# Optimization experiments

Measured on AMD Instinct MI355X. Metric: run time of the kernel, lower is better.

The kernel has to match this reference:

```python
import jax, jax.numpy as jnp
import numpy as np

E = 8       # n_experts
K = 2       # k_experts
D_IN = 1024
D_OUT = 1024
D_EXP = 2048
N = 16384   # tokens (batch*seq, forward requires 2D input)


def setup_inputs() -> dict:
    key = jax.random.key(0)
    ks = jax.random.split(key, 4)
    x = jax.random.normal(ks[0], (N, D_IN), jnp.float32)
    Wg = jax.random.normal(ks[1], (E, D_IN), jnp.float32) * 0.02      # router weight
    bg = jnp.zeros((E,), jnp.float32)                                  # router bias
    W_in = jax.random.normal(ks[2], (E, D_EXP, D_IN), jnp.float32) * 0.02
    b_in = jnp.zeros((E, D_EXP), jnp.float32)                          # w_in_bias_init=0.0
    W_out = jax.random.normal(ks[3], (E, D_OUT, D_EXP), jnp.float32) * 0.02  # bias=False
    return {"x": x, "Wg": Wg, "bg": bg, "W_in": W_in, "b_in": b_in, "W_out": W_out}


def moe_forward(x, Wg, bg, W_in, b_in, W_out):
    # Eval mode: gate jitter / solu jitter / dropouts are training-only no-ops.
    n = x.shape[0]
    # --- routing ---
    logits = x @ Wg.T + bg                                 # [N, E]
    probs = jax.nn.softmax(logits, axis=-1)
    mean_probs = probs.mean(axis=0)                        # [E]
    k_vals, k_idx = jax.lax.top_k(probs, K)                # [N, K]
    k_w = k_vals / k_vals.sum(axis=-1, keepdims=True)      # renormalized gate weights
    counts = jnp.bincount(k_idx.reshape(-1), length=E)     # [E] int
    load_balancing_loss = E * jnp.sum((counts.astype(x.dtype) / n) * mean_probs)
    # --- dispatch + expert w_in (loop over fixed small E; combine with one-hot mask) ---
    sel = jax.nn.one_hot(k_idx, E, dtype=x.dtype)          # [N, K, E]
    h = jnp.zeros((n, K, D_EXP), x.dtype)                  # preacts per (token, slot)
    for e in range(E):
        he = x @ W_in[e].T + b_in[e]                       # [N, D_EXP]
        h = h + sel[:, :, e][..., None] * he[:, None, :]
    # --- SoLU (eval): softmax(preacts) * preacts over hidden dim ---
    acts = jax.nn.softmax(h, axis=-1) * h                  # [N, K, D_EXP]
    # --- expert w_out (no bias) ---
    out = jnp.zeros((n, K, D_OUT), x.dtype)
    for e in range(E):
        oe = jnp.einsum('nkh,oh->nko', acts, W_out[e])
        out = out + sel[:, :, e][..., None] * oe
    # --- weighted combine over the K chosen experts ---
    outputs = (out * k_w[..., None]).sum(axis=1)           # [N, D_OUT]
    return outputs, load_balancing_loss


def reference(x, Wg, bg, W_in, b_in, W_out):
    return moe_forward(x, Wg, bg, W_in, b_in, W_out)
```

## Files before the change

### kernel.cpp

```cpp
#include <hip/hip_runtime.h>
#include <hip/hip_bf16.h>
#include <stdint.h>

#define E_EXP 8
#define NTOK  16384
#define DIN   1024
#define DEXP  2048
#define DOUT  1024
#define NSLOT (NTOK*2)
#define MAXT  264

#define AS_T  (128*64)
#define BS_T  (256*64)

typedef __attribute__((ext_vector_type(8))) short short8;
typedef __attribute__((ext_vector_type(8))) unsigned short ushort8;
typedef __attribute__((ext_vector_type(4))) unsigned short ushort4v;
typedef __attribute__((ext_vector_type(4))) float f32x4;

__device__ __forceinline__ unsigned short f2bf(float f){
  union { float f; uint32_t u; } v; v.f = f;
  uint32_t r = (v.u + 0x7FFFu + ((v.u >> 16) & 1u)) >> 16;
  return (unsigned short)r;
}
__device__ __forceinline__ float bf2f(unsigned short u){
  union { uint32_t u; float f; } v; v.u = ((uint32_t)u) << 16;
  return v.f;
}

__device__ __forceinline__ void async16(const void* g, void* l){
  __builtin_amdgcn_global_load_lds(
      (const __attribute__((address_space(1))) void*)g,
      (__attribute__((address_space(3))) void*)l, 16, 0, 0);
}

#define VMCNT12() asm volatile("s_waitcnt vmcnt(12)" ::: "memory")
#define VMCNT6()  asm volatile("s_waitcnt vmcnt(6)"  ::: "memory")
#define VMCNT0()  asm volatile("s_waitcnt vmcnt(0)"  ::: "memory")
#define BARRIER() do { asm volatile("" ::: "memory"); __builtin_amdgcn_s_barrier(); asm volatile("" ::: "memory"); } while(0)

__global__ __launch_bounds__(256) void cast2(const float* __restrict__ a,
                                             const float* __restrict__ b,
                                             unsigned short* __restrict__ da,
                                             unsigned short* __restrict__ db,
                                             int na, int nb){
  int i = (blockIdx.x*256 + threadIdx.x)*8;
  const float* s; unsigned short* d;
  if (i < na){ s = a + i; d = da + i; }
  else { int j = i - na; if (j >= nb) return; s = b + j; d = db + j; }
  float4 x = *(const float4*)(s);
  float4 y = *(const float4*)(s+4);
  ushort8 o;
  o[0]=f2bf(x.x); o[1]=f2bf(x.y); o[2]=f2bf(x.z); o[3]=f2bf(x.w);
  o[4]=f2bf(y.x); o[5]=f2bf(y.y); o[6]=f2bf(y.z); o[7]=f2bf(y.w);
  *(ushort8*)d = o;
}

__global__ __launch_bounds__(256) void router(
    const float* __restrict__ x, const float* __restrict__ Wg, const float* __restrict__ bg,
    unsigned short* __restrict__ xb,
    int* __restrict__ eidx, float* __restrict__ gw,
    int* __restrict__ counts, float* __restrict__ probsum)
{
  __shared__ float sWg[E_EXP*DIN];
  __shared__ float sps[E_EXP];
  __shared__ int   scnt[E_EXP];
  const int tid = threadIdx.x;
  for (int i = tid; i < E_EXP*DIN; i += 256) sWg[i] = Wg[i];
  if (tid < E_EXP){ sps[tid]=0.f; scnt[tid]=0; }
  __syncthreads();
  const int lane = tid & 63;
  const int wv   = tid >> 6;
  for (int it = 0; it < 16; ++it){
    const int token = blockIdx.x*64 + wv*16 + it;
    float4 xv[4];
#pragma unroll
    for (int j=0;j<4;++j) xv[j] = *(const float4*)&x[(size_t)token*DIN + j*256 + lane*4];
#pragma unroll
    for (int j=0;j<4;++j){
      ushort4v o;
      o[0]=f2bf(xv[j].x); o[1]=f2bf(xv[j].y); o[2]=f2bf(xv[j].z); o[3]=f2bf(xv[j].w);
      *(ushort4v*)&xb[(size_t)token*DIN + j*256 + lane*4] = o;
    }
    float p[E_EXP];
#pragma unroll
    for (int e2=0;e2<E_EXP;++e2){
      float s = 0.f;
#pragma unroll
      for (int j=0;j<4;++j){
        const float4 w4 = *(const float4*)&sWg[e2*DIN + j*256 + lane*4];
        s += xv[j].x*w4.x + xv[j].y*w4.y + xv[j].z*w4.z + xv[j].w*w4.w;
      }
      p[e2] = s;
    }
#pragma unroll
    for (int d=1; d<64; d<<=1){
#pragma unroll
      for (int e2=0;e2<E_EXP;++e2) p[e2] += __shfl_xor(p[e2], d);
    }
    if (lane == 0){
      float mx = -1e30f;
#pragma unroll
      for (int e2=0;e2<E_EXP;++e2){ p[e2] += bg[e2]; mx = fmaxf(mx, p[e2]); }
      float se = 0.f;
#pragma unroll
      for (int e2=0;e2<E_EXP;++e2){ p[e2] = __expf(p[e2]-mx); se += p[e2]; }
      const float inv = 1.f/se;
#pragma unroll
      for (int e2=0;e2<E_EXP;++e2){ p[e2] *= inv; atomicAdd(&sps[e2], p[e2]); }
      int i1 = 0;
#pragma unroll
      for (int e2=1;e2<E_EXP;++e2) if (p[e2] > p[i1]) i1 = e2;
      int i2 = (i1==0) ? 1 : 0;
#pragma unroll
      for (int e2=0;e2<E_EXP;++e2) if (e2 != i1 && p[e2] > p[i2]) i2 = e2;
      const float v1 = p[i1], v2 = p[i2], s12 = v1 + v2;
      eidx[2*token]   = i1; eidx[2*token+1] = i2;
      gw[2*token]     = v1/s12; gw[2*token+1] = v2/s12;
      atomicAdd(&scnt[i1], 1); atomicAdd(&scnt[i2], 1);
    }
  }
  __syncthreads();
  if (tid < E_EXP){ atomicAdd(&counts[tid], scnt[tid]); atomicAdd(&probsum[tid], sps[tid]); }
}

__global__ void finalize(const int* __restrict__ counts, const float* __restrict__ probsum,
                         float* __restrict__ loss_out, int* __restrict__ offs,
                         int* __restrict__ cursor, int* __restrict__ tile_e,
                         int* __restrict__ tile_row, int* __restrict__ ntiles)
{
  const int lane = threadIdx.x;
  int c[E_EXP];
#pragma unroll
  for (int e=0;e<E_EXP;++e) c[e] = counts[e];
  int off[E_EXP+1], tb[E_EXP+1];
  off[0]=0; tb[0]=0;
#pragma unroll
  for (int e=0;e<E_EXP;++e){ off[e+1]=off[e]+c[e]; tb[e+1]=tb[e]+((c[e]+127)>>7); }
  if (lane==0){
    float loss=0.f;
#pragma unroll
    for (int e=0;e<E_EXP;++e) loss += (float)c[e]*probsum[e];
    *loss_out = loss * (8.f/((float)NTOK*(float)NTOK));
    *ntiles = tb[E_EXP];
    offs[E_EXP] = off[E_EXP];
  }
  if (lane < E_EXP){ cursor[lane]=0; offs[lane]=off[lane]; }
  const int nt = tb[E_EXP];
  for (int i=lane; i<nt; i+=64){
    int e=0;
#pragma unroll
    for (int k=0;k<E_EXP-1;++k) if (i >= tb[k+1]) e = k+1;
    tile_e[i]   = e;
    tile_row[i] = off[e] + (i - tb[e])*128;
  }
}

__global__ __launch_bounds__(256) void scatter(const int* __restrict__ eidx,
    const int* __restrict__ offs, int* __restrict__ cursor,
    int* __restrict__ ptok, int* __restrict__ inv)
{
  const int t = blockIdx.x*256 + threadIdx.x;
  if (t >= NTOK) return;
#pragma unroll
  for (int s=0;s<2;++s){
    const int e2  = eidx[2*t+s];
    const int pos = offs[e2] + atomicAdd(&cursor[e2], 1);
    ptok[pos] = t;
    inv[2*t+s] = pos;
  }
}

__global__ __launch_bounds__(512, 2) void gemm1(
    const unsigned short* __restrict__ xb,
    const unsigned short* __restrict__ wib,
    const float* __restrict__ b_in,
    unsigned short* __restrict__ H,
    const int* __restrict__ ptok,
    const int* __restrict__ offs,
    const int* __restrict__ tile_e,
    const int* __restrict__ tile_row,
    const int* __restrict__ ntiles)
{
  if ((int)blockIdx.y >= *ntiles) return;
  const int e    = tile_e[blockIdx.y];
  const int row0 = tile_row[blockIdx.y];
  const int seg_end = offs[e+1];
  const int col0 = blockIdx.x * 256;

  __shared__ unsigned short As[3*AS_T];
  __shared__ unsigned short Bs[3*BS_T];

  const int tid  = threadIdx.x;
  const int lane = tid & 63;
  const int wv   = tid >> 6;
  const int wm   = wv >> 2;
  const int wn   = wv & 3;
  const int srow = tid >> 3;
  const int scol = ((tid & 7) ^ (srow & 7)) * 8;

  const unsigned short* ag[2];
#pragma unroll
  for (int i = 0; i < 2; ++i){
    int g = row0 + i*64 + srow; if (g > NSLOT-1) g = NSLOT-1;
    const int tok = ptok[g];
    ag[i] = xb + (size_t)tok*DIN + scol;
  }
  const unsigned short* bg4[4];
#pragma unroll
  for (int i = 0; i < 4; ++i)
    bg4[i] = wib + ((size_t)e*DEXP + col0 + i*64 + srow)*DIN + scol;
  float bias[4];
#pragma unroll
  for (int n = 0; n < 4; ++n)
    bias[n] = b_in[e*DEXP + col0 + wn*64 + n*16 + (lane&15)];

  f32x4 acc[4][4] = {};
  const int NK = DIN/64;

  const unsigned int aL0 = (wv*8)*64, aL1 = (64 + wv*8)*64;
  const unsigned int bL0 = (wv*8)*64, bL1 = (64+wv*8)*64, bL2 = (128+wv*8)*64, bL3 = (192+wv*8)*64;

#pragma unroll
  for (int t0 = 0; t0 < 2; ++t0){
    const int ko = t0*64;
    async16(ag[0]  + ko, &As[t0*AS_T + aL0]);
    async16(ag[1]  + ko, &As[t0*AS_T + aL1]);
    async16(bg4[0] + ko, &Bs[t0*BS_T + bL0]);
    async16(bg4[1] + ko, &Bs[t0*BS_T + bL1]);
    async16(bg4[2] + ko, &Bs[t0*BS_T + bL2]);
    async16(bg4[3] + ko, &Bs[t0*BS_T + bL3]);
  }

  int cur = 0, stg = 2;
  for (int kt = 0; kt < NK; ++kt){
    BARRIER();
    if (kt + 2 < NK){
      const int ko = (kt+2)*64;
      async16(ag[0]  + ko, &As[stg*AS_T + aL0]);
      async16(ag[1]  + ko, &As[stg*AS_T + aL1]);
      async16(bg4[0] + ko, &Bs[stg*BS_T + bL0]);
      async16(bg4[1] + ko, &Bs[stg*BS_T + bL1]);
      async16(bg4[2] + ko, &Bs[stg*BS_T + bL2]);
      async16(bg4[3] + ko, &Bs[stg*BS_T + bL3]);
      VMCNT12();
    } else if (kt + 1 < NK){
      VMCNT6();
    } else {
      VMCNT0();
    }
    BARRIER();

    const unsigned short* Ab = &As[cur*AS_T];
    const unsigned short* Bb = &Bs[cur*BS_T];
    __builtin_amdgcn_s_setprio(1);
#pragma unroll
    for (int kk = 0; kk < 2; ++kk){
      const int ksl = ((kk*4 + (lane>>4)) ^ (lane & 7)) * 8;
      short8 a[4], b[4];
#pragma unroll
      for (int m = 0; m < 4; ++m)
        a[m] = *(const short8*)&Ab[(wm*64 + m*16 + (lane&15))*64 + ksl];
#pragma unroll
      for (int n = 0; n < 4; ++n)
        b[n] = *(const short8*)&Bb[(wn*64 + n*16 + (lane&15))*64 + ksl];
#pragma unroll
      for (int m = 0; m < 4; ++m)
#pragma unroll
        for (int n = 0; n < 4; ++n)
          acc[m][n] = __builtin_amdgcn_mfma_f32_16x16x32_bf16(a[m], b[n], acc[m][n], 0, 0, 0);
    }
    __builtin_amdgcn_s_setprio(0);
    cur = (cur == 2) ? 0 : cur + 1;
    stg = (stg == 2) ? 0 : stg + 1;
  }

#pragma unroll
  for (int m = 0; m < 4; ++m){
#pragma unroll
    for (int j = 0; j < 4; ++j){
      const int r = wm*64 + m*16 + (lane>>4)*4 + j;
      const int g = row0 + r;
      if (g < seg_end){
#pragma unroll
        for (int n = 0; n < 4; ++n){
          const int c = col0 + wn*64 + n*16 + (lane&15);
          H[(size_t)g*DEXP + c] = f2bf(acc[m][n][j] + bias[n]);
        }
      }
    }
  }
}

__global__ __launch_bounds__(256) void solu(unsigned short* __restrict__ H){
  const size_t row = blockIdx.x;
  unsigned short* hp = H + row*DEXP;
  const int tid  = threadIdx.x;
  const int lane = tid & 63;
  const int wv   = tid >> 6;
  const short8 hv = *(const short8*)&hp[tid*8];
  float f[8];
#pragma unroll
  for (int j=0;j<8;++j) f[j] = bf2f((unsigned short)hv[j]);
  float mx = f[0];
#pragma unroll
  for (int j=1;j<8;++j) mx = fmaxf(mx, f[j]);
  for (int d=1; d<64; d<<=1) mx = fmaxf(mx, __shfl_xor(mx, d));
  __shared__ float redm[4];
  __shared__ float reds[4];
  if (lane==0) redm[wv] = mx;
  __syncthreads();
  mx = fmaxf(fmaxf(redm[0],redm[1]), fmaxf(redm[2],redm[3]));
  float se = 0.f; float ex[8];
#pragma unroll
  for (int j=0;j<8;++j){ ex[j] = __expf(f[j]-mx); se += ex[j]; }
  for (int d=1; d<64; d<<=1) se += __shfl_xor(se, d);
  if (lane==0) reds[wv] = se;
  __syncthreads();
  se = reds[0]+reds[1]+reds[2]+reds[3];
  const float inv = 1.0f/se;
  ushort8 o;
#pragma unroll
  for (int j=0;j<8;++j) o[j] = f2bf(f[j]*ex[j]*inv);
  *(ushort8*)&hp[tid*8] = o;
}

__global__ __launch_bounds__(512, 2) void gemm2(
    const unsigned short* __restrict__ ACT,
    const unsigned short* __restrict__ wob,
    unsigned short* __restrict__ Oslot,
    const int* __restrict__ offs,
    const int* __restrict__ tile_e,
    const int* __restrict__ tile_row,
    const int* __restrict__ ntiles)
{
  if ((int)blockIdx.y >= *ntiles) return;
  const int e    = tile_e[blockIdx.y];
  const int row0 = tile_row[blockIdx.y];
  const int seg_end = offs[e+1];
  const int col0 = blockIdx.x * 256;

  __shared__ unsigned short As[3*AS_T];
  __shared__ unsigned short Bs[3*BS_T];

  const int tid  = threadIdx.x;
  const int lane = tid & 63;
  const int wv   = tid >> 6;
  const int wm   = wv >> 2;
  const int wn   = wv & 3;
  const int srow = tid >> 3;
  const int scol = ((tid & 7) ^ (srow & 7)) * 8;

  const unsigned short* ag[2];
#pragma unroll
  for (int i = 0; i < 2; ++i){
    int g = row0 + i*64 + srow; if (g > NSLOT-1) g = NSLOT-1;
    ag[i] = ACT + (size_t)g*DEXP + scol;
  }
  const unsigned short* bg4[4];
#pragma unroll
  for (int i = 0; i < 4; ++i)
    bg4[i] = wob + ((size_t)e*DOUT + col0 + i*64 + srow)*DEXP + scol;

  f32x4 acc[4][4] = {};
  const int NK = DEXP/64;

  const unsigned int aL0 = (wv*8)*64, aL1 = (64 + wv*8)*64;
  const unsigned int bL0 = (wv*8)*64, bL1 = (64+wv*8)*64, bL2 = (128+wv*8)*64, bL3 = (192+wv*8)*64;

#pragma unroll
  for (int t0 = 0; t0 < 2; ++t0){
    const int ko = t0*64;
    async16(ag[0]  + ko, &As[t0*AS_T + aL0]);
    async16(ag[1]  + ko, &As[t0*AS_T + aL1]);
    async16(bg4[0] + ko, &Bs[t0*BS_T + bL0]);
    async16(bg4[1] + ko, &Bs[t0*BS_T + bL1]);
    async16(bg4[2] + ko, &Bs[t0*BS_T + bL2]);
    async16(bg4[3] + ko, &Bs[t0*BS_T + bL3]);
  }

  int cur = 0, stg = 2;
  for (int kt = 0; kt < NK; ++kt){
    BARRIER();
    if (kt + 2 < NK){
      const int ko = (kt+2)*64;
      async16(ag[0]  + ko, &As[stg*AS_T + aL0]);
      async16(ag[1]  + ko, &As[stg*AS_T + aL1]);
      async16(bg4[0] + ko, &Bs[stg*BS_T + bL0]);
      async16(bg4[1] + ko, &Bs[stg*BS_T + bL1]);
      async16(bg4[2] + ko, &Bs[stg*BS_T + bL2]);
      async16(bg4[3] + ko, &Bs[stg*BS_T + bL3]);
      VMCNT12();
    } else if (kt + 1 < NK){
      VMCNT6();
    } else {
      VMCNT0();
    }
    BARRIER();

    const unsigned short* Ab = &As[cur*AS_T];
    const unsigned short* Bb = &Bs[cur*BS_T];
    __builtin_amdgcn_s_setprio(1);
#pragma unroll
    for (int kk = 0; kk < 2; ++kk){
      const int ksl = ((kk*4 + (lane>>4)) ^ (lane & 7)) * 8;
      short8 a[4], b[4];
#pragma unroll
      for (int m = 0; m < 4; ++m)
        a[m] = *(const short8*)&Ab[(wm*64 + m*16 + (lane&15))*64 + ksl];
#pragma unroll
      for (int n = 0; n < 4; ++n)
        b[n] = *(const short8*)&Bb[(wn*64 + n*16 + (lane&15))*64 + ksl];
#pragma unroll
      for (int m = 0; m < 4; ++m)
#pragma unroll
        for (int n = 0; n < 4; ++n)
          acc[m][n] = __builtin_amdgcn_mfma_f32_16x16x32_bf16(a[m], b[n], acc[m][n], 0, 0, 0);
    }
    __builtin_amdgcn_s_setprio(0);
    cur = (cur == 2) ? 0 : cur + 1;
    stg = (stg == 2) ? 0 : stg + 1;
  }

#pragma unroll
  for (int m = 0; m < 4; ++m){
#pragma unroll
    for (int j = 0; j < 4; ++j){
      const int r = wm*64 + m*16 + (lane>>4)*4 + j;
      const int g = row0 + r;
      if (g < seg_end){
#pragma unroll
        for (int n = 0; n < 4; ++n){
          const int c = col0 + wn*64 + n*16 + (lane&15);
          Oslot[(size_t)g*DOUT + c] = f2bf(acc[m][n][j]);
        }
      }
    }
  }
}

__global__ __launch_bounds__(256) void combine(const unsigned short* __restrict__ Oslot,
    const int* __restrict__ inv, const float* __restrict__ gw, float* __restrict__ out)
{
  const int t    = blockIdx.x*4 + (threadIdx.x >> 6);
  const int lane = threadIdx.x & 63;
  const int p0 = inv[2*t], p1 = inv[2*t+1];
  const float w0 = gw[2*t], w1 = gw[2*t+1];
  const unsigned short* r0 = Oslot + (size_t)p0*DOUT + lane*16;
  const unsigned short* r1 = Oslot + (size_t)p1*DOUT + lane*16;
  ushort8 a0 = *(const ushort8*)r0;
  ushort8 a1 = *(const ushort8*)(r0 + 8);
  ushort8 b0 = *(const ushort8*)r1;
  ushort8 b1 = *(const ushort8*)(r1 + 8);
  float* op = out + (size_t)t*DOUT + lane*16;
  float4 o;
#pragma unroll
  for (int q = 0; q < 2; ++q){
    const ushort8 ua = q ? a1 : a0;
    const ushort8 ub = q ? b1 : b0;
#pragma unroll
    for (int h = 0; h < 2; ++h){
      o.x = w0*bf2f(ua[h*4+0]) + w1*bf2f(ub[h*4+0]);
      o.y = w0*bf2f(ua[h*4+1]) + w1*bf2f(ub[h*4+1]);
      o.z = w0*bf2f(ua[h*4+2]) + w1*bf2f(ub[h*4+2]);
      o.w = w0*bf2f(ua[h*4+3]) + w1*bf2f(ub[h*4+3]);
      *(float4*)(op + q*8 + h*4) = o;
    }
  }
}

extern "C" void kernel_launch(void* const* d_in, const int* in_sizes, int n_in,
                              void* d_out, int out_size, void* d_ws, size_t ws_size,
                              hipStream_t stream)
{
  const float* x     = (const float*)d_in[0];
  const float* Wg    = (const float*)d_in[1];
  const float* bgp   = (const float*)d_in[2];
  const float* W_in  = (const float*)d_in[3];
  const float* b_in  = (const float*)d_in[4];
  const float* W_out = (const float*)d_in[5];
  float* out = (float*)d_out;

  char* base = (char*)d_ws;
  size_t o = 0;
  unsigned short* xb  = (unsigned short*)(base + o); o += (size_t)NTOK*DIN*2;
  unsigned short* wib = (unsigned short*)(base + o); o += (size_t)E_EXP*DEXP*DIN*2;
  unsigned short* wob = (unsigned short*)(base + o); o += (size_t)E_EXP*DOUT*DEXP*2;
  unsigned short* H   = (unsigned short*)(base + o); o += (size_t)NSLOT*DEXP*2;
  unsigned short* Oslot = (unsigned short*)d_ws;
  int*   eidx    = (int*)(base + o);   o += (size_t)NSLOT*4;
  float* gw      = (float*)(base + o); o += (size_t)NSLOT*4;
  int*   ptok    = (int*)(base + o);   o += (size_t)NSLOT*4;
  int*   inv     = (int*)(base + o);   o += (size_t)NSLOT*4;
  int*   counts  = (int*)(base + o);   o += 32;
  float* probsum = (float*)(base + o); o += 32;
  int*   cursor  = (int*)(base + o);   o += 32;
  int*   offs    = (int*)(base + o);   o += 64;
  int*   tile_e  = (int*)(base + o);   o += (size_t)MAXT*4;
  int*   tile_row= (int*)(base + o);   o += (size_t)MAXT*4;
  int*   ntiles  = (int*)(base + o);   o += 64;

  hipMemsetAsync(counts, 0, 96, stream);

  cast2<<<dim3(16384), 256, 0, stream>>>(W_in, W_out, wib, wob,
                                         E_EXP*DEXP*DIN, E_EXP*DOUT*DEXP);

  router<<<dim3(256), 256, 0, stream>>>(x, Wg, bgp, xb, eidx, gw, counts, probsum);
  finalize<<<dim3(1), 64, 0, stream>>>(counts, probsum, out + (size_t)NTOK*DOUT,
                                       offs, cursor, tile_e, tile_row, ntiles);
  scatter<<<dim3(64), 256, 0, stream>>>(eidx, offs, cursor, ptok, inv);

  gemm1<<<dim3(DEXP/256, MAXT), 512, 0, stream>>>(xb, wib, b_in, H, ptok, offs,
                                                  tile_e, tile_row, ntiles);
  solu<<<dim3(NSLOT), 256, 0, stream>>>(H);
  gemm2<<<dim3(DOUT/256, MAXT), 512, 0, stream>>>(H, wob, Oslot, offs,
                                                  tile_e, tile_row, ntiles);
  combine<<<dim3(NTOK/4), 256, 0, stream>>>(Oslot, inv, gw, out);
}
```

Before: 857.3 us.

## Enlarge expert GEMM tiles to 256x256 with double-buffered LDS pipeline

Both grouped expert GEMMs move from 128x256 to 256x256 output tiles, so each wave computes 128x64 with 8x4 MFMA accumulators and each loaded B tile is reused across twice as many rows. To fit LDS, the three-stage async prefetch becomes a two-stage double buffer and the occupancy hint of two blocks per CU is dropped. Routing tile bookkeeping now rounds segments to 256 rows. The intent is higher arithmetic intensity and fewer weight reloads, at the cost of more register pressure, lower occupancy, a shallower pipeline, and more padding waste per expert segment.

After: 769.9 us. 10.2% less time.

```diff
diff --git a/kernel.cpp b/kernel.cpp
--- a/kernel.cpp
+++ b/kernel.cpp
@@ -8,10 +8,9 @@
 #define DEXP  2048
 #define DOUT  1024
 #define NSLOT (NTOK*2)
-#define MAXT  264
-
-#define AS_T  (128*64)
-#define BS_T  (256*64)
+#define MAXT  136
+
+#define TS_T  (256*64)
 
 typedef __attribute__((ext_vector_type(8))) short short8;
 typedef __attribute__((ext_vector_type(8))) unsigned short ushort8;
@@ -34,8 +33,7 @@
       (__attribute__((address_space(3))) void*)l, 16, 0, 0);
 }
 
-#define VMCNT12() asm volatile("s_waitcnt vmcnt(12)" ::: "memory")
-#define VMCNT6()  asm volatile("s_waitcnt vmcnt(6)"  ::: "memory")
+#define VMCNT8()  asm volatile("s_waitcnt vmcnt(8)"  ::: "memory")
 #define VMCNT0()  asm volatile("s_waitcnt vmcnt(0)"  ::: "memory")
 #define BARRIER() do { asm volatile("" ::: "memory"); __builtin_amdgcn_s_barrier(); asm volatile("" ::: "memory"); } while(0)
 
@@ -136,7 +134,7 @@
   int off[E_EXP+1], tb[E_EXP+1];
   off[0]=0; tb[0]=0;
 #pragma unroll
-  for (int e=0;e<E_EXP;++e){ off[e+1]=off[e]+c[e]; tb[e+1]=tb[e]+((c[e]+127)>>7); }
+  for (int e=0;e<E_EXP;++e){ off[e+1]=off[e]+c[e]; tb[e+1]=tb[e]+((c[e]+255)>>8); }
   if (lane==0){
     float loss=0.f;
 #pragma unroll
@@ -152,7 +150,7 @@
 #pragma unroll
     for (int k=0;k<E_EXP-1;++k) if (i >= tb[k+1]) e = k+1;
     tile_e[i]   = e;
-    tile_row[i] = off[e] + (i - tb[e])*128;
+    tile_row[i] = off[e] + (i - tb[e])*256;
   }
 }
 
@@ -171,7 +169,7 @@
   }
 }
 
-__global__ __launch_bounds__(512, 2) void gemm1(
+__global__ __launch_bounds__(512) void gemm1(
     const unsigned short* __restrict__ xb,
     const unsigned short* __restrict__ wib,
     const float* __restrict__ b_in,
@@ -188,8 +186,8 @@
   const int seg_end = offs[e+1];
   const int col0 = blockIdx.x * 256;
 
-  __shared__ unsigned short As[3*AS_T];
-  __shared__ unsigned short Bs[3*BS_T];
+  __shared__ unsigned short As[2][TS_T];
+  __shared__ unsigned short Bs[2][TS_T];
 
   const int tid  = threadIdx.x;
   const int lane = tid & 63;
@@ -199,9 +197,9 @@
   const int srow = tid >> 3;
   const int scol = ((tid & 7) ^ (srow & 7)) * 8;
 
-  const unsigned short* ag[2];
-#pragma unroll
-  for (int i = 0; i < 2; ++i){
+  const unsigned short* ag[4];
+#pragma unroll
+  for (int i = 0; i < 4; ++i){
     int g = row0 + i*64 + srow; if (g > NSLOT-1) g = NSLOT-1;
     const int tok = ptok[g];
     ag[i] = xb + (size_t)tok*DIN + scol;
@@ -215,71 +213,57 @@
   for (int n = 0; n < 4; ++n)
     bias[n] = b_in[e*DEXP + col0 + wn*64 + n*16 + (lane&15)];
 
-  f32x4 acc[4][4] = {};
+  f32x4 acc[8][4] = {};
   const int NK = DIN/64;
-
-  const unsigned int aL0 = (wv*8)*64, aL1 = (64 + wv*8)*64;
-  const unsigned int bL0 = (wv*8)*64, bL1 = (64+wv*8)*64, bL2 = (128+wv*8)*64, bL3 = (192+wv*8)*64;
-
-#pragma unroll
-  for (int t0 = 0; t0 < 2; ++t0){
-    const int ko = t0*64;
-    async16(ag[0]  + ko, &As[t0*AS_T + aL0]);
-    async16(ag[1]  + ko, &As[t0*AS_T + aL1]);
-    async16(bg4[0] + ko, &Bs[t0*BS_T + bL0]);
-    async16(bg4[1] + ko, &Bs[t0*BS_T + bL1]);
-    async16(bg4[2] + ko, &Bs[t0*BS_T + bL2]);
-    async16(bg4[3] + ko, &Bs[t0*BS_T + bL3]);
-  }
-
-  int cur = 0, stg = 2;
+  int cur = 0;
+
+  const unsigned int L0 = (wv*8)*64, L1 = (64+wv*8)*64, L2o = (128+wv*8)*64, L3 = (192+wv*8)*64;
+
+  async16(ag[0],  &As[0][L0]);  async16(ag[1],  &As[0][L1]);
+  async16(ag[2],  &As[0][L2o]); async16(ag[3],  &As[0][L3]);
+  async16(bg4[0], &Bs[0][L0]);  async16(bg4[1], &Bs[0][L1]);
+  async16(bg4[2], &Bs[0][L2o]); async16(bg4[3], &Bs[0][L3]);
+
   for (int kt = 0; kt < NK; ++kt){
     BARRIER();
-    if (kt + 2 < NK){
-      const int ko = (kt+2)*64;
-      async16(ag[0]  + ko, &As[stg*AS_T + aL0]);
-      async16(ag[1]  + ko, &As[stg*AS_T + aL1]);
-      async16(bg4[0] + ko, &Bs[stg*BS_T + bL0]);
-      async16(bg4[1] + ko, &Bs[stg*BS_T + bL1]);
-      async16(bg4[2] + ko, &Bs[stg*BS_T + bL2]);
-      async16(bg4[3] + ko, &Bs[stg*BS_T + bL3]);
-      VMCNT12();
-    } else if (kt + 1 < NK){
-      VMCNT6();
+    if (kt + 1 < NK){
+      const int ko = (kt+1)*64;
+      async16(ag[0]  + ko, &As[cur^1][L0]);  async16(ag[1]  + ko, &As[cur^1][L1]);
+      async16(ag[2]  + ko, &As[cur^1][L2o]); async16(ag[3]  + ko, &As[cur^1][L3]);
+      async16(bg4[0] + ko, &Bs[cur^1][L0]);  async16(bg4[1] + ko, &Bs[cur^1][L1]);
+      async16(bg4[2] + ko, &Bs[cur^1][L2o]); async16(bg4[3] + ko, &Bs[cur^1][L3]);
+      VMCNT8();
     } else {
       VMCNT0();
     }
     BARRIER();
 
-    const unsigned short* Ab = &As[cur*AS_T];
-    const unsigned short* Bb = &Bs[cur*BS_T];
     __builtin_amdgcn_s_setprio(1);
 #pragma unroll
     for (int kk = 0; kk < 2; ++kk){
       const int ksl = ((kk*4 + (lane>>4)) ^ (lane & 7)) * 8;
-      short8 a[4], b[4];
-#pragma unroll
-      for (int m = 0; m < 4; ++m)
-        a[m] = *(const short8*)&Ab[(wm*64 + m*16 + (lane&15))*64 + ksl];
+      short8 a[8], b[4];
+#pragma unroll
+      for (int m = 0; m < 8; ++m)
+        a[m] = *(const short8*)&As[cur][(wm*128 + m*16 + (lane&15))*64 + ksl];
 #pragma unroll
       for (int n = 0; n < 4; ++n)
-        b[n] = *(const short8*)&Bb[(wn*64 + n*16 + (lane&15))*64 + ksl];
-#pragma unroll
-      for (int m = 0; m < 4; ++m)
+        b[n] = *(const short8*)&Bs[cur][(wn*64 + n*16 + (lane&15))*64 + ksl];
+#pragma unroll
+      for (int m = 0; m < 8; ++m)
 #pragma unroll
         for (int n = 0; n < 4; ++n)
           acc[m][n] = __builtin_amdgcn_mfma_f32_16x16x32_bf16(a[m], b[n], acc[m][n], 0, 0, 0);
     }
     __builtin_amdgcn_s_setprio(0);
-    cur = (cur == 2) ? 0 : cur + 1;
-    stg = (stg == 2) ? 0 : stg + 1;
-  }
-
-#pragma unroll
-  for (int m = 0; m < 4; ++m){
+    cur ^= 1;
+  }
+
+#pragma unroll
+  for (int m = 0; m < 8; ++m){
 #pragma unroll
     for (int j = 0; j < 4; ++j){
-      const int r = wm*64 + m*16 + (lane>>4)*4 + j;
+      const int r = wm*128 + m*16 + (lane>>4)*4 + j;
       const int g = row0 + r;
       if (g < seg_end){
 #pragma unroll
@@ -325,7 +309,7 @@
   *(ushort8*)&hp[tid*8] = o;
 }
 
-__global__ __launch_bounds__(512, 2) void gemm2(
+__global__ __launch_bounds__(512) void gemm2(
     const unsigned short* __restrict__ ACT,
     const unsigned short* __restrict__ wob,
     unsigned short* __restrict__ Oslot,
@@ -340,8 +324,8 @@
   const int seg_end = offs[e+1];
   const int col0 = blockIdx.x * 256;
 
-  __shared__ unsigned short As[3*AS_T];
-  __shared__ unsigned short Bs[3*BS_T];
+  __shared__ unsigned short As[2][TS_T];
+  __shared__ unsigned short Bs[2][TS_T];
 
   const int tid  = threadIdx.x;
   const int lane = tid & 63;
@@ -351,9 +335,9 @@
   const int srow = tid >> 3;
   const int scol = ((tid & 7) ^ (srow & 7)) * 8;
 
-  const unsigned short* ag[2];
-#pragma unroll
-  for (int i = 0; i < 2; ++i){
+  const unsigned short* ag[4];
+#pragma unroll
+  for (int i = 0; i < 4; ++i){
     int g = row0 + i*64 + srow; if (g > NSLOT-1) g = NSLOT-1;
     ag[i] = ACT + (size_t)g*DEXP + scol;
   }
@@ -362,71 +346,57 @@
   for (int i = 0; i < 4; ++i)
     bg4[i] = wob + ((size_t)e*DOUT + col0 + i*64 + srow)*DEXP + scol;
 
-  f32x4 acc[4][4] = {};
+  f32x4 acc[8][4] = {};
   const int NK = DEXP/64;
-
-  const unsigned int aL0 = (wv*8)*64, aL1 = (64 + wv*8)*64;
-  const unsigned int bL0 = (wv*8)*64, bL1 = (64+wv*8)*64, bL2 = (128+wv*8)*64, bL3 = (192+wv*8)*64;
-
-#pragma unroll
-  for (int t0 = 0; t0 < 2; ++t0){
-    const int ko = t0*64;
-    async16(ag[0]  + ko, &As[t0*AS_T + aL0]);
-    async16(ag[1]  + ko, &As[t0*AS_T + aL1]);
-    async16(bg4[0] + ko, &Bs[t0*BS_T + bL0]);
-    async16(bg4[1] + ko, &Bs[t0*BS_T + bL1]);
-    async16(bg4[2] + ko, &Bs[t0*BS_T + bL2]);
-    async16(bg4[3] + ko, &Bs[t0*BS_T + bL3]);
-  }
-
-  int cur = 0, stg = 2;
+  int cur = 0;
+
+  const unsigned int L0 = (wv*8)*64, L1 = (64+wv*8)*64, L2o = (128+wv*8)*64, L3 = (192+wv*8)*64;
+
+  async16(ag[0],  &As[0][L0]);  async16(ag[1],  &As[0][L1]);
+  async16(ag[2],  &As[0][L2o]); async16(ag[3],  &As[0][L3]);
+  async16(bg4[0], &Bs[0][L0]);  async16(bg4[1], &Bs[0][L1]);
+  async16(bg4[2], &Bs[0][L2o]); async16(bg4[3], &Bs[0][L3]);
+
   for (int kt = 0; kt < NK; ++kt){
     BARRIER();
-    if (kt + 2 < NK){
-      const int ko = (kt+2)*64;
-      async16(ag[0]  + ko, &As[stg*AS_T + aL0]);
-      async16(ag[1]  + ko, &As[stg*AS_T + aL1]);
-      async16(bg4[0] + ko, &Bs[stg*BS_T + bL0]);
-      async16(bg4[1] + ko, &Bs[stg*BS_T + bL1]);
-      async16(bg4[2] + ko, &Bs[stg*BS_T + bL2]);
-      async16(bg4[3] + ko, &Bs[stg*BS_T + bL3]);
-      VMCNT12();
-    } else if (kt + 1 < NK){
-      VMCNT6();
+    if (kt + 1 < NK){
+      const int ko = (kt+1)*64;
+      async16(ag[0]  + ko, &As[cur^1][L0]);  async16(ag[1]  + ko, &As[cur^1][L1]);
+      async16(ag[2]  + ko, &As[cur^1][L2o]); async16(ag[3]  + ko, &As[cur^1][L3]);
+      async16(bg4[0] + ko, &Bs[cur^1][L0]);  async16(bg4[1] + ko, &Bs[cur^1][L1]);
+      async16(bg4[2] + ko, &Bs[cur^1][L2o]); async16(bg4[3] + ko, &Bs[cur^1][L3]);
+      VMCNT8();
     } else {
       VMCNT0();
     }
     BARRIER();
 
-    const unsigned short* Ab = &As[cur*AS_T];
-    const unsigned short* Bb = &Bs[cur*BS_T];
     __builtin_amdgcn_s_setprio(1);
 #pragma unroll
     for (int kk = 0; kk < 2; ++kk){
       const int ksl = ((kk*4 + (lane>>4)) ^ (lane & 7)) * 8;
-      short8 a[4], b[4];
-#pragma unroll
-      for (int m = 0; m < 4; ++m)
-        a[m] = *(const short8*)&Ab[(wm*64 + m*16 + (lane&15))*64 + ksl];
+      short8 a[8], b[4];
+#pragma unroll
+      for (int m = 0; m < 8; ++m)
+        a[m] = *(const short8*)&As[cur][(wm*128 + m*16 + (lane&15))*64 + ksl];
 #pragma unroll
       for (int n = 0; n < 4; ++n)
-        b[n] = *(const short8*)&Bb[(wn*64 + n*16 + (lane&15))*64 + ksl];
-#pragma unroll
-      for (int m = 0; m < 4; ++m)
+        b[n] = *(const short8*)&Bs[cur][(wn*64 + n*16 + (lane&15))*64 + ksl];
+#pragma unroll
+      for (int m = 0; m < 8; ++m)
 #pragma unroll
         for (int n = 0; n < 4; ++n)
           acc[m][n] = __builtin_amdgcn_mfma_f32_16x16x32_bf16(a[m], b[n], acc[m][n], 0, 0, 0);
     }
     __builtin_amdgcn_s_setprio(0);
-    cur = (cur == 2) ? 0 : cur + 1;
-    stg = (stg == 2) ? 0 : stg + 1;
-  }
-
-#pragma unroll
-  for (int m = 0; m < 4; ++m){
+    cur ^= 1;
+  }
+
+#pragma unroll
+  for (int m = 0; m < 8; ++m){
 #pragma unroll
     for (int j = 0; j < 4; ++j){
-      const int r = wm*64 + m*16 + (lane>>4)*4 + j;
+      const int r = wm*128 + m*16 + (lane>>4)*4 + j;
       const int g = row0 + r;
       if (g < seg_end){
 #pragma unroll
```
